# Optimization experiments

Measured on AMD Instinct MI355X. Metric: run time of the kernel, lower is better.

Reference implementation:

```python
import jax, jax.numpy as jnp
import numpy as np

B, N, D, H, FF, K, L = 8, 4096, 128, 8, 512, 16, 2
DH = D // H
EPS = 1e-5


def setup_inputs() -> dict:
    key = jax.random.key(0)
    ks = jax.random.split(key, 32)
    s = 0.02
    inp = {
        "x": jax.random.normal(ks[0], (B, N, 8), dtype=jnp.float32),
        "xyz_w": jax.random.normal(ks[1], (D, 3), jnp.float32) * s,
        "xyz_b": jnp.zeros((D,), jnp.float32),
        "ohe_w": jax.random.normal(ks[2], (D, 5), jnp.float32) * s,
        "ohe_b": jnp.zeros((D,), jnp.float32),
        # per-layer transformer params stacked on leading L axis
        "in_proj_w": jax.random.normal(ks[3], (L, 3 * D, D), jnp.float32) * s,
        "in_proj_b": jnp.zeros((L, 3 * D), jnp.float32),
        "out_proj_w": jax.random.normal(ks[4], (L, D, D), jnp.float32) * s,
        "out_proj_b": jnp.zeros((L, D), jnp.float32),
        "ln1_w": jnp.ones((L, D), jnp.float32),
        "ln1_b": jnp.zeros((L, D), jnp.float32),
        "lin1_w": jax.random.normal(ks[5], (L, FF, D), jnp.float32) * s,
        "lin1_b": jnp.zeros((L, FF), jnp.float32),
        "lin2_w": jax.random.normal(ks[6], (L, D, FF), jnp.float32) * s,
        "lin2_b": jnp.zeros((L, D), jnp.float32),
        "ln2_w": jnp.ones((L, D), jnp.float32),
        "ln2_b": jnp.zeros((L, D), jnp.float32),
        "fc1_w": jax.random.normal(ks[7], (FF, D), jnp.float32) * s,
        "fc1_b": jnp.zeros((FF,), jnp.float32),
        "fc2_w": jax.random.normal(ks[8], (1, FF), jnp.float32) * s,
        "fc2_b": jnp.zeros((1,), jnp.float32),
    }
    return inp


def _layer_norm(x, w, b):
    m = jnp.mean(x, -1, keepdims=True)
    v = jnp.mean((x - m) ** 2, -1, keepdims=True)
    return (x - m) * jax.lax.rsqrt(v + EPS) * w + b


def _knn_attention(xyz, feat):
    # squared euclidean distances preserve top-k ordering of cdist(p=2)
    d2 = jnp.sum((xyz[:, :, None, :] - xyz[:, None, :, :]) ** 2, -1)  # [B,N,N]
    _, idx = jax.lax.top_k(-d2, K + 1)  # ascending distance
    idx = idx[..., 1:]  # drop self -> [B,N,K]
    knn = jax.vmap(lambda f, i: f[i])(feat, idx)  # [B,N,K,D]
    scale = 1.0 / np.sqrt(D)
    scores = jnp.einsum('bnd,bnkd->bnk', feat, knn) * scale
    w = jax.nn.softmax(scores, -1)
    return jnp.einsum('bnk,bnkd->bnd', w, knn)


def _mha(x, in_w, in_b, out_w, out_b):
    qkv = x @ in_w.T + in_b  # [B,N,3D]
    q, k, v = jnp.split(qkv, 3, axis=-1)
    def heads(t):
        return t.reshape(B, N, H, DH).transpose(0, 2, 1, 3)  # [B,H,N,DH]
    q, k, v = heads(q), heads(k), heads(v)
    scores = jnp.einsum('bhqd,bhkd->bhqk', q, k) / np.sqrt(DH)
    a = jax.nn.softmax(scores, -1)
    o = jnp.einsum('bhqk,bhkd->bhqd', a, v).transpose(0, 2, 1, 3).reshape(B, N, D)
    return o @ out_w.T + out_b


def reference(x, xyz_w, xyz_b, ohe_w, ohe_b, in_proj_w, in_proj_b, out_proj_w,
              out_proj_b, ln1_w, ln1_b, lin1_w, lin1_b, lin2_w, lin2_b,
              ln2_w, ln2_b, fc1_w, fc1_b, fc2_w, fc2_b):
    xyz = x[:, :, :3]
    ohe = x[:, :, 3:8]
    feat = (xyz @ xyz_w.T + xyz_b) + (ohe @ ohe_w.T + ohe_b)  # [B,N,D]
    h = _knn_attention(xyz, feat)
    # post-norm TransformerEncoder (PyTorch default, relu, no dropout at eval)
    for l in range(L):
        a = _mha(h, in_proj_w[l], in_proj_b[l], out_proj_w[l], out_proj_b[l])
        h = _layer_norm(h + a, ln1_w[l], ln1_b[l])
        f = jax.nn.relu(h @ lin1_w[l].T + lin1_b[l]) @ lin2_w[l].T + lin2_b[l]
        h = _layer_norm(h + f, ln2_w[l], ln2_b[l])
    pooled = jnp.mean(h, axis=1)  # [B,D]
    out = jax.nn.sigmoid(jax.nn.relu(pooled @ fc1_w.T + fc1_b) @ fc2_w.T + fc2_b)
    return out
```

## Files before the change

### kernel.cpp

```cpp
#include <hip/hip_runtime.h>

#define Bq 8
#define Nq 4096
#define Dq 128
#define Hq 8
#define FFq 512
#define KNNq 16
#define Lq 2
#define DHq 16
#define EPSq 1e-5f

typedef _Float16 half4 __attribute__((ext_vector_type(4)));
typedef _Float16 half2t __attribute__((ext_vector_type(2)));
typedef float v4f __attribute__((ext_vector_type(4)));

static __device__ __forceinline__ half2t pkrtz(float a, float b) {
    return __builtin_bit_cast(half2t, __builtin_amdgcn_cvt_pkrtz(a, b));
}

__global__ __launch_bounds__(256) void prep_kernel(const float* __restrict__ x,
                                                   const float* __restrict__ xyz_w,
                                                   const float* __restrict__ xyz_b,
                                                   const float* __restrict__ ohe_w,
                                                   const float* __restrict__ ohe_b,
                                                   _Float16* __restrict__ feat16,
                                                   const float* __restrict__ ipw,
                                                   const float* __restrict__ opw,
                                                   const float* __restrict__ l1w,
                                                   const float* __restrict__ l2w,
                                                   _Float16* __restrict__ wb) {
    int bid = blockIdx.x;
    if (bid < 16384) {
        int i = bid * 256 + threadIdx.x;
        int d = i & 127;
        int t = i >> 7;
        const float* xr = x + (size_t)t * 8;
        float s = xyz_b[d] + ohe_b[d];
        s += xr[0] * xyz_w[d * 3 + 0] + xr[1] * xyz_w[d * 3 + 1] + xr[2] * xyz_w[d * 3 + 2];
        s += xr[3] * ohe_w[d * 5 + 0] + xr[4] * ohe_w[d * 5 + 1] + xr[5] * ohe_w[d * 5 + 2]
           + xr[6] * ohe_w[d * 5 + 3] + xr[7] * ohe_w[d * 5 + 4];
        feat16[i] = (_Float16)s;
    } else {
        int i = (bid - 16384) * 256 + threadIdx.x;
        float v;
        if (i < 98304) v = ipw[i];
        else if (i < 131072) v = opw[i - 98304];
        else if (i < 262144) v = l1w[i - 131072];
        else v = l2w[i - 262144];
        wb[i] = (_Float16)v;
    }
}

__global__ __launch_bounds__(512) void knn_kernel(const float* __restrict__ x, int* __restrict__ idx) {
    __shared__ __attribute__((aligned(16))) float sx[Nq];
    __shared__ __attribute__((aligned(16))) float sy[Nq];
    __shared__ __attribute__((aligned(16))) float sz[Nq];
    unsigned int (*md)[17] = (unsigned int (*)[17])sx;
    int b = blockIdx.y;
    int tid = threadIdx.x;
    for (int p = tid; p < Nq; p += 512) {
        const float* xr = x + ((size_t)b * Nq + p) * 8;
        sx[p] = xr[0]; sy[p] = xr[1]; sz[p] = xr[2];
    }
    __syncthreads();
    int qi = tid >> 3;
    int part = tid & 7;
    int n = blockIdx.x * 64 + qi;
    float qx = sx[n], qy = sy[n], qz = sz[n];
    unsigned int bdA[KNNq], bdB[KNNq];
#pragma unroll
    for (int i = 0; i < KNNq; i++) { bdA[i] = 0xFFFFFFFFu; bdB[i] = 0xFFFFFFFFu; }
    int j0 = part * 512;
    int rot = part;
    for (int jj = 0; jj < 256; jj++) {
        int j1 = j0 + ((jj + rot) & 511);
        int j2 = j0 + ((jj + 256 + rot) & 511);
        float p1x = sx[j1], p1y = sy[j1], p1z = sz[j1];
        float p2x = sx[j2], p2y = sy[j2], p2z = sz[j2];
        float dx1 = qx - p1x, dy1 = qy - p1y, dz1 = qz - p1z;
        float dx2 = qx - p2x, dy2 = qy - p2y, dz2 = qz - p2z;
        float d21 = fmaf(dx1, dx1, fmaf(dy1, dy1, dz1 * dz1));
        float d22 = fmaf(dx2, dx2, fmaf(dy2, dy2, dz2 * dz2));
        unsigned int k1 = (__float_as_uint(d21) & 0xFFFFF000u) | (unsigned int)j1;
        unsigned int k2 = (__float_as_uint(d22) & 0xFFFFF000u) | (unsigned int)j2;
        k1 = (j1 == n) ? 0xFFFFFFFFu : k1;
        k2 = (j2 == n) ? 0xFFFFFFFFu : k2;
#pragma unroll
        for (int i = 0; i < KNNq; i++) {
            unsigned int loA = bdA[i] < k1 ? bdA[i] : k1;
            unsigned int hiA = bdA[i] < k1 ? k1 : bdA[i];
            bdA[i] = loA; k1 = hiA;
            unsigned int loB = bdB[i] < k2 ? bdB[i] : k2;
            unsigned int hiB = bdB[i] < k2 ? k2 : bdB[i];
            bdB[i] = loB; k2 = hiB;
        }
    }
#pragma unroll
    for (int t = 0; t < KNNq; t++) {
        unsigned int key = bdB[t];
#pragma unroll
        for (int i = 0; i < KNNq; i++) {
            unsigned int lo = bdA[i] < key ? bdA[i] : key;
            unsigned int hi = bdA[i] < key ? key : bdA[i];
            bdA[i] = lo; key = hi;
        }
    }
    __syncthreads();
#pragma unroll
    for (int i = 0; i < KNNq; i++) md[tid][i] = bdA[i];
    __syncthreads();
    if (part == 0) {
        unsigned int pall = 0;
        int* op = idx + ((size_t)b * Nq + n) * KNNq;
        int base_row = qi * 8;
#pragma unroll
        for (int s = 0; s < KNNq; s++) {
            unsigned int best = 0xFFFFFFFFu; int bp = 0;
#pragma unroll
            for (int p2 = 0; p2 < 8; p2++) {
                unsigned int ptr = (pall >> (p2 * 4)) & 15u;
                unsigned int v = md[base_row + p2][ptr];
                if (v < best) { best = v; bp = p2; }
            }
            op[s] = (int)(best & 4095u);
            pall += (1u << (bp * 4));
        }
    }
}

__global__ __launch_bounds__(256, 4) void knn_attn_kernel(const _Float16* __restrict__ feat16,
                                                          const int* __restrict__ idx,
                                                          _Float16* __restrict__ h16) {
    int wave = threadIdx.x >> 6;
    int lane = threadIdx.x & 63;
    int token = blockIdx.x * 4 + wave;
    int b = token >> 12;
    half2t fh = ((const half2t*)(feat16 + (size_t)token * Dq))[lane];
    float2 f = make_float2((float)fh[0], (float)fh[1]);
    const int* ip = idx + (size_t)token * KNNq;
    int jj[KNNq];
#pragma unroll
    for (int k = 0; k < KNNq; k++) jj[k] = ip[k];
    float2 g[KNNq];
#pragma unroll
    for (int k = 0; k < KNNq; k++) {
        half2t gh = ((const half2t*)(feat16 + (((size_t)b << 12) + jj[k]) * Dq))[lane];
        g[k] = make_float2((float)gh[0], (float)gh[1]);
    }
    float sc[KNNq];
#pragma unroll
    for (int k = 0; k < KNNq; k++) {
        float p = f.x * g[k].x + f.y * g[k].y;
#pragma unroll
        for (int m = 1; m < 64; m <<= 1) p += __shfl_xor(p, m);
        sc[k] = p * 0.088388347648318447f;
    }
    float mx = sc[0];
#pragma unroll
    for (int k = 1; k < KNNq; k++) mx = fmaxf(mx, sc[k]);
    float sum = 0.f;
#pragma unroll
    for (int k = 0; k < KNNq; k++) { sc[k] = __expf(sc[k] - mx); sum += sc[k]; }
    float inv = 1.f / sum;
    float o0 = 0.f, o1 = 0.f;
#pragma unroll
    for (int k = 0; k < KNNq; k++) { o0 += sc[k] * g[k].x; o1 += sc[k] * g[k].y; }
    ((half2t*)(h16 + (size_t)token * Dq))[lane] = pkrtz(o0 * inv, o1 * inv);
}

template <int MODE>
__global__ __launch_bounds__(256) void hgemm_kernel(const _Float16* __restrict__ A,
                                                    const _Float16* __restrict__ W,
                                                    const float* __restrict__ bias,
                                                    void* __restrict__ Cout,
                                                    int M, int Nc, int K) {
    int tid = threadIdx.x;
    int lane = tid & 63, w = tid >> 6;
    int l15 = lane & 15, l4 = lane >> 4;
    int m0 = blockIdx.y * 64 + w * 16;
    int n0 = blockIdx.x * 64;
    const _Float16* Ap = A + (size_t)(m0 + l15) * K + l4 * 4;
    const _Float16* Wp = W + (size_t)(n0 + l15) * K + l4 * 4;
    v4f acc[4] = {{0.f, 0.f, 0.f, 0.f}, {0.f, 0.f, 0.f, 0.f}, {0.f, 0.f, 0.f, 0.f}, {0.f, 0.f, 0.f, 0.f}};
    for (int ks = 0; ks < K; ks += 16) {
        half4 af = *(const half4*)(Ap + ks);
#pragma unroll
        for (int nt = 0; nt < 4; nt++) {
            half4 wf = *(const half4*)(Wp + (size_t)nt * 16 * K + ks);
            acc[nt] = __builtin_amdgcn_mfma_f32_16x16x16f16(wf, af, acc[nt], 0, 0, 0);
        }
    }
    int m = m0 + l15;
#pragma unroll
    for (int nt = 0; nt < 4; nt++) {
        int nb = n0 + nt * 16 + l4 * 4;
        float4 bv = *(const float4*)(bias + nb);
        float v0 = acc[nt][0] + bv.x, v1 = acc[nt][1] + bv.y;
        float v2 = acc[nt][2] + bv.z, v3 = acc[nt][3] + bv.w;
        int n_base = n0 + nt * 16;
        int sel = n_base >> 7;
        if (MODE == 2 && sel == 0) {
            v0 *= 0.36067376f; v1 *= 0.36067376f; v2 *= 0.36067376f; v3 *= 0.36067376f;
        }
        half2t lo = pkrtz(v0, v1);
        half2t hi = pkrtz(v2, v3);
        half4 hv; hv[0] = lo[0]; hv[1] = lo[1]; hv[2] = hi[0]; hv[3] = hi[1];
        if (sel < 2) {
            int hh = (n_base >> 4) & 7;
            size_t base = (size_t)sel * (64ull * Nq * 16)
                        + ((size_t)((m >> 12) * 8 + hh)) * (Nq * 16)
                        + (size_t)(m & 4095) * 16 + l4 * 4;
            *(half4*)((_Float16*)Cout + base) = hv;
        } else {
            int hh = (n_base >> 4) & 7;
            size_t vb = 2ull * 64 * Nq * 16
                      + ((size_t)((m >> 12) * 8 + hh)) * (16 * Nq)
                      + (size_t)(m & 4095);
            _Float16* vp = (_Float16*)Cout + vb + (size_t)(l4 * 4) * Nq;
            vp[0 * Nq] = hv[0]; vp[1 * Nq] = hv[1]; vp[2 * Nq] = hv[2]; vp[3 * Nq] = hv[3];
        }
    }
}

__global__ __launch_bounds__(256) void flash9_kernel(const _Float16* __restrict__ pk,
                                                     _Float16* __restrict__ out16) {
    __shared__ _Float16 Ks[2][64 * 20];
    __shared__ _Float16 Vs[2][16 * 66];
    int tid = threadIdx.x;
    int lane = tid & 63, w = tid >> 6;
    int bh = blockIdx.y;
    const _Float16* Qb = pk + (size_t)bh * (Nq * 16);
    const _Float16* Kb = pk + (size_t)(64 + bh) * (Nq * 16);
    const _Float16* Vt = pk + 2ull * 64 * Nq * 16 + (size_t)bh * (16 * Nq);
    int q0 = blockIdx.x * 64 + w * 16;
    int l15 = lane & 15, l4 = lane >> 4;

    half4 qf = *(const half4*)(Qb + (size_t)(q0 + l15) * 16 + l4 * 4);

    int sr = tid >> 2, sc = tid & 3;
    int vd = tid >> 4, vj = (tid & 15) * 4;
    const _Float16* Kg = Kb + (size_t)sr * 16 + sc * 4;
    const _Float16* Vg = Vt + (size_t)vd * Nq + vj;

    *(half4*)(Ks[0] + sr * 20 + sc * 4) = *(const half4*)(Kg);
    *(half4*)(Vs[0] + vd * 66 + vj) = *(const half4*)(Vg);
    __syncthreads();

    v4f o = {0.f, 0.f, 0.f, 0.f};
    float lsum = 0.f;

    for (int kt = 0; kt < Nq / 64; kt++) {
        int cur = kt & 1, nxt = cur ^ 1;
        if (kt < Nq / 64 - 1) {
            *(half4*)(Ks[nxt] + sr * 20 + sc * 4) = *(const half4*)(Kg + (size_t)(kt + 1) * 64 * 16);
            *(half4*)(Vs[nxt] + vd * 66 + vj) = *(const half4*)(Vg + (kt + 1) * 64);
        }
        v4f S[4];
#pragma unroll
        for (int g = 0; g < 4; g++) {
            half4 kf = *(const half4*)(Ks[cur] + (g * 16 + l15) * 20 + l4 * 4);
            S[g] = __builtin_amdgcn_mfma_f32_16x16x16f16(kf, qf, (v4f){0.f, 0.f, 0.f, 0.f}, 0, 0, 0);
        }
        half4 P[4];
#pragma unroll
        for (int g = 0; g < 4; g++) {
            float p0 = __builtin_amdgcn_exp2f(S[g][0]);
            float p1 = __builtin_amdgcn_exp2f(S[g][1]);
            float p2 = __builtin_amdgcn_exp2f(S[g][2]);
            float p3 = __builtin_amdgcn_exp2f(S[g][3]);
            lsum += (p0 + p1) + (p2 + p3);
            half2t lo = pkrtz(p0, p1);
            half2t hi = pkrtz(p2, p3);
            P[g][0] = lo[0]; P[g][1] = lo[1]; P[g][2] = hi[0]; P[g][3] = hi[1];
        }
#pragma unroll
        for (int g = 0; g < 4; g++) {
            half4 vf = *(const half4*)(Vs[cur] + l15 * 66 + g * 16 + l4 * 4);
            o = __builtin_amdgcn_mfma_f32_16x16x16f16(vf, P[g], o, 0, 0, 0);
        }
        __syncthreads();
    }
    lsum += __shfl_xor(lsum, 16);
    lsum += __shfl_xor(lsum, 32);
    float inv = 1.f / lsum;
    int row = q0 + l15;
    int b = bh >> 3, hh = bh & 7;
    half2t lo = pkrtz(o[0] * inv, o[1] * inv);
    half2t hi = pkrtz(o[2] * inv, o[3] * inv);
    half4 hv; hv[0] = lo[0]; hv[1] = lo[1]; hv[2] = hi[0]; hv[3] = hi[1];
    *(half4*)(out16 + ((size_t)(b * Nq + row)) * Dq + hh * 16 + l4 * 4) = hv;
}

__global__ __launch_bounds__(256) void hgemm_ln_kernel(const _Float16* __restrict__ A,
                                                       const _Float16* __restrict__ W,
                                                       const float* __restrict__ bias,
                                                       const float* __restrict__ lnw,
                                                       const float* __restrict__ lnb,
                                                       _Float16* __restrict__ h16,
                                                       int K) {
    int tid = threadIdx.x;
    int lane = tid & 63, w = tid >> 6;
    int l15 = lane & 15, l4 = lane >> 4;
    int m0 = blockIdx.x * 64 + w * 16;
    const _Float16* Ap = A + (size_t)(m0 + l15) * K + l4 * 4;
    const _Float16* Wp = W + (size_t)l15 * K + l4 * 4;
    v4f acc[8] = {};
    for (int ks = 0; ks < K; ks += 16) {
        half4 af = *(const half4*)(Ap + ks);
#pragma unroll
        for (int nt = 0; nt < 8; nt++) {
            half4 wf = *(const half4*)(Wp + (size_t)nt * 16 * K + ks);
            acc[nt] = __builtin_amdgcn_mfma_f32_16x16x16f16(wf, af, acc[nt], 0, 0, 0);
        }
    }
    int m = m0 + l15;
    float x[8][4];
    float psum = 0.f;
#pragma unroll
    for (int nt = 0; nt < 8; nt++) {
        int nb = nt * 16 + l4 * 4;
        float4 bv = *(const float4*)(bias + nb);
        half4 rv = *(const half4*)(h16 + (size_t)m * Dq + nb);
        x[nt][0] = acc[nt][0] + bv.x + (float)rv[0];
        x[nt][1] = acc[nt][1] + bv.y + (float)rv[1];
        x[nt][2] = acc[nt][2] + bv.z + (float)rv[2];
        x[nt][3] = acc[nt][3] + bv.w + (float)rv[3];
        psum += (x[nt][0] + x[nt][1]) + (x[nt][2] + x[nt][3]);
    }
    psum += __shfl_xor(psum, 16);
    psum += __shfl_xor(psum, 32);
    float mean = psum * (1.f / 128.f);
    float vsum = 0.f;
#pragma unroll
    for (int nt = 0; nt < 8; nt++)
#pragma unroll
        for (int r = 0; r < 4; r++) {
            x[nt][r] -= mean;
            vsum += x[nt][r] * x[nt][r];
        }
    vsum += __shfl_xor(vsum, 16);
    vsum += __shfl_xor(vsum, 32);
    float inv = rsqrtf(vsum * (1.f / 128.f) + EPSq);
#pragma unroll
    for (int nt = 0; nt < 8; nt++) {
        int nb = nt * 16 + l4 * 4;
        float4 wv = *(const float4*)(lnw + nb);
        float4 bb = *(const float4*)(lnb + nb);
        float y0 = x[nt][0] * inv * wv.x + bb.x;
        float y1 = x[nt][1] * inv * wv.y + bb.y;
        float y2 = x[nt][2] * inv * wv.z + bb.z;
        float y3 = x[nt][3] * inv * wv.w + bb.w;
        half2t lo = pkrtz(y0, y1);
        half2t hi = pkrtz(y2, y3);
        half4 hv2; hv2[0] = lo[0]; hv2[1] = lo[1]; hv2[2] = hi[0]; hv2[3] = hi[1];
        *(half4*)(h16 + (size_t)m * Dq + nb) = hv2;
    }
}

template <int LAST>
__global__ __launch_bounds__(256) void ffn_kernel(const _Float16* __restrict__ h16in,
                                                  const _Float16* __restrict__ W1,
                                                  const float* __restrict__ b1,
                                                  const _Float16* __restrict__ W2,
                                                  const float* __restrict__ b2,
                                                  const float* __restrict__ lnw,
                                                  const float* __restrict__ lnb,
                                                  _Float16* __restrict__ h16,
                                                  float* __restrict__ part) {
    int tid = threadIdx.x;
    int lane = tid & 63, w = tid >> 6;
    int l15 = lane & 15, l4 = lane >> 4;
    int m0 = blockIdx.x * 64 + w * 16;
    int m = m0 + l15;
    const _Float16* Ap = h16in + (size_t)m * Dq + l4 * 4;
    half4 afr[8];
#pragma unroll
    for (int t = 0; t < 8; t++) afr[t] = *(const half4*)(Ap + t * 16);
    half4 mid[32];
#pragma unroll
    for (int c = 0; c < 8; c++) {
        v4f acc[4] = {};
#pragma unroll
        for (int t = 0; t < 8; t++) {
#pragma unroll
            for (int nt = 0; nt < 4; nt++) {
                half4 wf = *(const half4*)(W1 + (size_t)(c * 64 + nt * 16 + l15) * 128 + t * 16 + l4 * 4);
                acc[nt] = __builtin_amdgcn_mfma_f32_16x16x16f16(wf, afr[t], acc[nt], 0, 0, 0);
            }
        }
#pragma unroll
        for (int nt = 0; nt < 4; nt++) {
            float4 bv = *(const float4*)(b1 + c * 64 + nt * 16 + l4 * 4);
            float v0 = fmaxf(acc[nt][0] + bv.x, 0.f);
            float v1 = fmaxf(acc[nt][1] + bv.y, 0.f);
            float v2 = fmaxf(acc[nt][2] + bv.z, 0.f);
            float v3 = fmaxf(acc[nt][3] + bv.w, 0.f);
            half2t lo = pkrtz(v0, v1), hi = pkrtz(v2, v3);
            half4 hv; hv[0] = lo[0]; hv[1] = lo[1]; hv[2] = hi[0]; hv[3] = hi[1];
            mid[c * 4 + nt] = hv;
        }
    }
    v4f acc8[8] = {};
#pragma unroll 4
    for (int t = 0; t < 32; t++) {
#pragma unroll
        for (int nt = 0; nt < 8; nt++) {
            half4 wf = *(const half4*)(W2 + (size_t)(nt * 16 + l15) * 512 + t * 16 + l4 * 4);
            acc8[nt] = __builtin_amdgcn_mfma_f32_16x16x16f16(wf, mid[t], acc8[nt], 0, 0, 0);
        }
    }
    float x[8][4];
    float psum = 0.f;
#pragma unroll
    for (int nt = 0; nt < 8; nt++) {
        int nb = nt * 16 + l4 * 4;
        float4 bv = *(const float4*)(b2 + nb);
        x[nt][0] = acc8[nt][0] + bv.x + (float)afr[nt][0];
        x[nt][1] = acc8[nt][1] + bv.y + (float)afr[nt][1];
        x[nt][2] = acc8[nt][2] + bv.z + (float)afr[nt][2];
        x[nt][3] = acc8[nt][3] + bv.w + (float)afr[nt][3];
        psum += (x[nt][0] + x[nt][1]) + (x[nt][2] + x[nt][3]);
    }
    psum += __shfl_xor(psum, 16);
    psum += __shfl_xor(psum, 32);
    float mean = psum * (1.f / 128.f);
    float vsum = 0.f;
#pragma unroll
    for (int nt = 0; nt < 8; nt++)
#pragma unroll
        for (int r = 0; r < 4; r++) {
            x[nt][r] -= mean;
            vsum += x[nt][r] * x[nt][r];
        }
    vsum += __shfl_xor(vsum, 16);
    vsum += __shfl_xor(vsum, 32);
    float inv = rsqrtf(vsum * (1.f / 128.f) + EPSq);
#pragma unroll
    for (int nt = 0; nt < 8; nt++) {
        int nb = nt * 16 + l4 * 4;
        float4 wv = *(const float4*)(lnw + nb);
        float4 bb = *(const float4*)(lnb + nb);
        x[nt][0] = x[nt][0] * inv * wv.x + bb.x;
        x[nt][1] = x[nt][1] * inv * wv.y + bb.y;
        x[nt][2] = x[nt][2] * inv * wv.z + bb.z;
        x[nt][3] = x[nt][3] * inv * wv.w + bb.w;
        if (!LAST) {
            half2t lo = pkrtz(x[nt][0], x[nt][1]);
            half2t hi = pkrtz(x[nt][2], x[nt][3]);
            half4 hv2; hv2[0] = lo[0]; hv2[1] = lo[1]; hv2[2] = hi[0]; hv2[3] = hi[1];
            *(half4*)(h16 + (size_t)m * Dq + nb) = hv2;
        }
    }
    if (LAST) {
#pragma unroll
        for (int nt = 0; nt < 8; nt++)
#pragma unroll
            for (int r = 0; r < 4; r++) {
                float v = x[nt][r];
                v += __shfl_xor(v, 1);
                v += __shfl_xor(v, 2);
                v += __shfl_xor(v, 4);
                v += __shfl_xor(v, 8);
                x[nt][r] = v;
            }
        if (l15 == 0) {
            float* pp = part + ((size_t)blockIdx.x * 4 + w) * Dq;
#pragma unroll
            for (int nt = 0; nt < 8; nt++)
#pragma unroll
                for (int r = 0; r < 4; r++)
                    pp[nt * 16 + l4 * 4 + r] = x[nt][r];
        }
    }
}

__global__ __launch_bounds__(512) void head_kernel(const float* __restrict__ part,
                                                   const float* __restrict__ fc1_w, const float* __restrict__ fc1_b,
                                                   const float* __restrict__ fc2_w, const float* __restrict__ fc2_b,
                                                   float* __restrict__ out) {
    __shared__ float psh[Dq];
    __shared__ float red[512];
    int b = blockIdx.x, f = threadIdx.x;
    if (f < Dq) {
        float s = 0.f;
        for (int c = 0; c < 256; c++) s += part[((size_t)b * 256 + c) * Dq + f];
        psh[f] = s * (1.f / 4096.f);
    }
    __syncthreads();
    const float* wr = fc1_w + (size_t)f * Dq;
    float s = fc1_b[f];
    for (int d = 0; d < Dq; d++) s += psh[d] * wr[d];
    red[f] = fmaxf(s, 0.f) * fc2_w[f];
    __syncthreads();
    for (int st = 256; st > 0; st >>= 1) {
        if (f < st) red[f] += red[f + st];
        __syncthreads();
    }
    if (f == 0) out[b] = 1.f / (1.f + __expf(-(red[0] + fc2_b[0])));
}

extern "C" void kernel_launch(void* const* d_in, const int* in_sizes, int n_in,
                              void* d_out, int out_size, void* d_ws, size_t ws_size,
                              hipStream_t stream) {
    const float* x        = (const float*)d_in[0];
    const float* xyz_w    = (const float*)d_in[1];
    const float* xyz_b    = (const float*)d_in[2];
    const float* ohe_w    = (const float*)d_in[3];
    const float* ohe_b    = (const float*)d_in[4];
    const float* in_proj_w  = (const float*)d_in[5];
    const float* in_proj_b  = (const float*)d_in[6];
    const float* out_proj_w = (const float*)d_in[7];
    const float* out_proj_b = (const float*)d_in[8];
    const float* ln1_w    = (const float*)d_in[9];
    const float* ln1_b    = (const float*)d_in[10];
    const float* lin1_w   = (const float*)d_in[11];
    const float* lin1_b   = (const float*)d_in[12];
    const float* lin2_w   = (const float*)d_in[13];
    const float* lin2_b   = (const float*)d_in[14];
    const float* ln2_w    = (const float*)d_in[15];
    const float* ln2_b    = (const float*)d_in[16];
    const float* fc1_w    = (const float*)d_in[17];
    const float* fc1_b    = (const float*)d_in[18];
    const float* fc2_w    = (const float*)d_in[19];
    const float* fc2_b    = (const float*)d_in[20];
    float* outp = (float*)d_out;

    char* ws = (char*)d_ws;
    size_t off = 0;
    auto alloc = [&](size_t bytes) { void* p = ws + off; off += (bytes + 255) & ~255ULL; return p; };
    _Float16*  feat16 = (_Float16*)alloc((size_t)Bq * Nq * Dq * 2);
    _Float16*  h16    = (_Float16*)alloc((size_t)Bq * Nq * Dq * 2);
    _Float16*  abuf16 = (_Float16*)alloc((size_t)Bq * Nq * Dq * 2);
    _Float16*  pkb    = (_Float16*)alloc(3ull * 64 * Nq * 16 * 2);
    _Float16*  wb     = (_Float16*)alloc(393216ull * 2);
    int*       idx    = (int*)alloc((size_t)Bq * Nq * KNNq * 4);
    float*     part   = (float*)alloc(2048ull * Dq * 4);
    if (off > ws_size) return;

    const _Float16* wip16 = wb;
    const _Float16* wop16 = wb + 98304;
    const _Float16* wl116 = wb + 131072;
    const _Float16* wl216 = wb + 262144;

    int M = Bq * Nq;

    prep_kernel<<<16384 + 1536, 256, 0, stream>>>(x, xyz_w, xyz_b, ohe_w, ohe_b, feat16,
                                                  in_proj_w, out_proj_w, lin1_w, lin2_w, wb);
    knn_kernel<<<dim3(Nq / 64, Bq), 512, 0, stream>>>(x, idx);
    knn_attn_kernel<<<M / 4, 256, 0, stream>>>(feat16, idx, h16);

    for (int l = 0; l < Lq; l++) {
        hgemm_kernel<2><<<dim3(384 / 64, M / 64), 256, 0, stream>>>(
            h16, wip16 + (size_t)l * 384 * 128, in_proj_b + l * 384, pkb, M, 384, 128);
        flash9_kernel<<<dim3(Nq / 64, Bq * Hq), 256, 0, stream>>>(pkb, abuf16);
        hgemm_ln_kernel<<<M / 64, 256, 0, stream>>>(
            abuf16, wop16 + (size_t)l * 128 * 128, out_proj_b + l * 128,
            ln1_w + l * 128, ln1_b + l * 128, h16, 128);
        if (l == 0) {
            ffn_kernel<0><<<M / 64, 256, 0, stream>>>(
                h16, wl116, lin1_b, wl216, lin2_b, ln2_w, ln2_b, h16, part);
        } else {
            ffn_kernel<1><<<M / 64, 256, 0, stream>>>(
                h16, wl116 + (size_t)l * 512 * 128, lin1_b + l * 512,
                wl216 + (size_t)l * 128 * 512, lin2_b + l * 128,
                ln2_w + l * 128, ln2_b + l * 128, h16, part);
        }
    }

    head_kernel<<<Bq, 512, 0, stream>>>(part, fc1_w, fc1_b, fc2_w, fc2_b, outp);
}
```

Baseline: 1.122 ms.

## Widen flash attention KV tile to 128 and compute row sums via MFMA

The attention kernel now stages 128 keys/values per iteration instead of 64, halving the number of loop iterations and barriers. The per-lane scalar softmax-denominator accumulation and final cross-lane shuffles are replaced by an extra MFMA that multiplies the probabilities by a ones matrix. Wave priority is also raised during the compute phase. The trade-off is double the LDS, more registers for the eight P fragments, and extra MFMA work for the sums, with fp16-rounded P used in the denominator.

Measured after the change: 1.861 ms. 65.9% more time.

```diff
diff --git a/kernel.cpp b/kernel.cpp
--- a/kernel.cpp
+++ b/kernel.cpp
@@ -222,10 +222,10 @@
     }
 }
 
-__global__ __launch_bounds__(256) void flash9_kernel(const _Float16* __restrict__ pk,
-                                                     _Float16* __restrict__ out16) {
-    __shared__ _Float16 Ks[2][64 * 20];
-    __shared__ _Float16 Vs[2][16 * 66];
+__global__ __launch_bounds__(256) void flash10_kernel(const _Float16* __restrict__ pk,
+                                                      _Float16* __restrict__ out16) {
+    __shared__ _Float16 Ks[2][128 * 20];
+    __shared__ _Float16 Vs[2][16 * 130];
     int tid = threadIdx.x;
     int lane = tid & 63, w = tid >> 6;
     int bh = blockIdx.y;
@@ -241,48 +241,61 @@
     int vd = tid >> 4, vj = (tid & 15) * 4;
     const _Float16* Kg = Kb + (size_t)sr * 16 + sc * 4;
     const _Float16* Vg = Vt + (size_t)vd * Nq + vj;
-
-    *(half4*)(Ks[0] + sr * 20 + sc * 4) = *(const half4*)(Kg);
-    *(half4*)(Vs[0] + vd * 66 + vj) = *(const half4*)(Vg);
+    _Float16* KsA = Ks[0] + sr * 20 + sc * 4;
+    _Float16* KsB = Ks[1] + sr * 20 + sc * 4;
+    _Float16* VsA = Vs[0] + vd * 130 + vj;
+    _Float16* VsB = Vs[1] + vd * 130 + vj;
+
+    *(half4*)(KsA) = *(const half4*)(Kg);
+    *(half4*)(KsA + 64 * 20) = *(const half4*)(Kg + 64 * 16);
+    *(half4*)(VsA) = *(const half4*)(Vg);
+    *(half4*)(VsA + 64) = *(const half4*)(Vg + 64);
     __syncthreads();
 
     v4f o = {0.f, 0.f, 0.f, 0.f};
-    float lsum = 0.f;
-
-    for (int kt = 0; kt < Nq / 64; kt++) {
-        int cur = kt & 1, nxt = cur ^ 1;
-        if (kt < Nq / 64 - 1) {
-            *(half4*)(Ks[nxt] + sr * 20 + sc * 4) = *(const half4*)(Kg + (size_t)(kt + 1) * 64 * 16);
-            *(half4*)(Vs[nxt] + vd * 66 + vj) = *(const half4*)(Vg + (kt + 1) * 64);
-        }
-        v4f S[4];
-#pragma unroll
-        for (int g = 0; g < 4; g++) {
-            half4 kf = *(const half4*)(Ks[cur] + (g * 16 + l15) * 20 + l4 * 4);
-            S[g] = __builtin_amdgcn_mfma_f32_16x16x16f16(kf, qf, (v4f){0.f, 0.f, 0.f, 0.f}, 0, 0, 0);
-        }
-        half4 P[4];
-#pragma unroll
-        for (int g = 0; g < 4; g++) {
-            float p0 = __builtin_amdgcn_exp2f(S[g][0]);
-            float p1 = __builtin_amdgcn_exp2f(S[g][1]);
-            float p2 = __builtin_amdgcn_exp2f(S[g][2]);
-            float p3 = __builtin_amdgcn_exp2f(S[g][3]);
-            lsum += (p0 + p1) + (p2 + p3);
+    v4f lac = {0.f, 0.f, 0.f, 0.f};
+    half4 ones;
+    ones[0] = ones[1] = ones[2] = ones[3] = (_Float16)1.0f;
+
+    const int NT = Nq / 128;
+    for (int kt = 0; kt < NT; kt++) {
+        int cur = kt & 1;
+        if (kt < NT - 1) {
+            const _Float16* kg = Kg + (size_t)(kt + 1) * (128 * 16);
+            const _Float16* vg = Vg + (kt + 1) * 128;
+            _Float16* kd = cur ? KsA : KsB;
+            _Float16* vdst = cur ? VsA : VsB;
+            *(half4*)(kd) = *(const half4*)(kg);
+            *(half4*)(kd + 64 * 20) = *(const half4*)(kg + 64 * 16);
+            *(half4*)(vdst) = *(const half4*)(vg);
+            *(half4*)(vdst + 64) = *(const half4*)(vg + 64);
+        }
+        const _Float16* Kc = cur ? Ks[1] : Ks[0];
+        const _Float16* Vc = cur ? Vs[1] : Vs[0];
+        __builtin_amdgcn_s_setprio(1);
+        half4 P[8];
+#pragma unroll
+        for (int g = 0; g < 8; g++) {
+            half4 kf = *(const half4*)(Kc + (g * 16 + l15) * 20 + l4 * 4);
+            v4f S = __builtin_amdgcn_mfma_f32_16x16x16f16(kf, qf, (v4f){0.f, 0.f, 0.f, 0.f}, 0, 0, 0);
+            float p0 = __builtin_amdgcn_exp2f(S[0]);
+            float p1 = __builtin_amdgcn_exp2f(S[1]);
+            float p2 = __builtin_amdgcn_exp2f(S[2]);
+            float p3 = __builtin_amdgcn_exp2f(S[3]);
             half2t lo = pkrtz(p0, p1);
             half2t hi = pkrtz(p2, p3);
             P[g][0] = lo[0]; P[g][1] = lo[1]; P[g][2] = hi[0]; P[g][3] = hi[1];
         }
 #pragma unroll
-        for (int g = 0; g < 4; g++) {
-            half4 vf = *(const half4*)(Vs[cur] + l15 * 66 + g * 16 + l4 * 4);
+        for (int g = 0; g < 8; g++) {
+            lac = __builtin_amdgcn_mfma_f32_16x16x16f16(ones, P[g], lac, 0, 0, 0);
+            half4 vf = *(const half4*)(Vc + l15 * 130 + g * 16 + l4 * 4);
             o = __builtin_amdgcn_mfma_f32_16x16x16f16(vf, P[g], o, 0, 0, 0);
         }
+        __builtin_amdgcn_s_setprio(0);
         __syncthreads();
     }
-    lsum += __shfl_xor(lsum, 16);
-    lsum += __shfl_xor(lsum, 32);
-    float inv = 1.f / lsum;
+    float inv = 1.f / lac[0];
     int row = q0 + l15;
     int b = bh >> 3, hh = bh & 7;
     half2t lo = pkrtz(o[0] * inv, o[1] * inv);
@@ -552,7 +565,7 @@
     for (int l = 0; l < Lq; l++) {
         hgemm_kernel<2><<<dim3(384 / 64, M / 64), 256, 0, stream>>>(
             h16, wip16 + (size_t)l * 384 * 128, in_proj_b + l * 384, pkb, M, 384, 128);
-        flash9_kernel<<<dim3(Nq / 64, Bq * Hq), 256, 0, stream>>>(pkb, abuf16);
+        flash10_kernel<<<dim3(Nq / 64, Bq * Hq), 256, 0, stream>>>(pkb, abuf16);
         hgemm_ln_kernel<<<M / 64, 256, 0, stream>>>(
             abuf16, wop16 + (size_t)l * 128 * 128, out_proj_b + l * 128,
             ln1_w + l * 128, ln1_b + l * 128, h16, 128);
```
